# Performance work log

Measured on AMD Instinct MI355X. Metric: run time of the kernel, lower is better.

The kernel has to match this reference:

```python
import jax, jax.numpy as jnp
import numpy as np

B, N, F, H, D = 4096, 14, 768, 1, 768  # batch, num_diseases, feature_dim, num_heads, hidden_dim
L = 3  # number of GAT layers


def setup_inputs() -> dict:
    key = jax.random.key(0)
    ks = jax.random.split(key, 8)
    features = jax.random.normal(ks[0], (B, N, F), dtype=jnp.float32)
    # random adjacency mask; ensure nonzero diagonal so no row is fully masked
    mask = (jax.random.uniform(ks[1], (B, N, N)) > 0.3).astype(jnp.float32)
    adj = jnp.maximum(mask, jnp.eye(N, dtype=jnp.float32))
    W_emb = jax.random.normal(ks[2], (F, D), dtype=jnp.float32) / np.sqrt(F)
    b_emb = jnp.zeros((D,), dtype=jnp.float32)
    gat_W = jax.random.normal(ks[3], (L, D, H * D), dtype=jnp.float32) / np.sqrt(D)
    gat_a = jax.random.normal(ks[4], (L, 2 * D, H), dtype=jnp.float32) / np.sqrt(2 * D)
    W_out = jax.random.normal(ks[5], (H * D, F), dtype=jnp.float32) / np.sqrt(H * D)
    b_out = jnp.zeros((F,), dtype=jnp.float32)
    return dict(features=features, adj=adj, W_emb=W_emb, b_emb=b_emb,
                gat_W=gat_W, gat_a=gat_a, W_out=W_out, b_out=b_out)


def _gat_layer(x, adj, W, a):
    # x: [B, N, D], W: [D, H*D], a: [2D, H]
    Bm, Nn = x.shape[0], x.shape[1]
    Wh = (x @ W).reshape(Bm, Nn, H, D)
    # e[b,i,j,h] = Wh[b,i,h] . a[:D,h] + Wh[b,j,h] . a[D:,h]  (concat attention, un-materialized)
    a_i, a_j = a[:D], a[D:]
    ei = jnp.einsum('bnhd,dh->bnh', Wh, a_i)
    ej = jnp.einsum('bnhd,dh->bnh', Wh, a_j)
    e = ei[:, :, None, :] + ej[:, None, :, :]  # [B, N, N, H]
    e = jnp.where(adj[..., None] > 0, e, jnp.float32(-1e30))  # masked_fill(-inf)
    attn = jax.nn.softmax(e, axis=2)  # softmax over j (dim=2), matches torch
    h = jnp.einsum('bijh,bjhd->bihd', attn, Wh)  # attention-weighted aggregation
    return h.reshape(Bm, Nn, H * D), attn  # concat=True output


def reference(features, adj, W_emb, b_emb, gat_W, gat_a, W_out, b_out):
    # dropout layers are identity at inference
    x = features @ W_emb + b_emb  # disease_embedding
    attns = []
    for l in range(L):
        x, attn = _gat_layer(x, adj, gat_W[l], gat_a[l])
        attns.append(attn)
        if l < L - 1:
            x = jax.nn.elu(x)
    out = x @ W_out + b_out  # output_proj
    return (out, attns[0], attns[1], attns[2])
```

## Files before the change

kernel.cpp:

```cpp
#include <hip/hip_runtime.h>

typedef unsigned short u16;
typedef float f32x4 __attribute__((ext_vector_type(4)));
typedef float f32x16 __attribute__((ext_vector_type(16)));
typedef short bf16x8 __attribute__((ext_vector_type(8)));
typedef unsigned short u16x8 __attribute__((ext_vector_type(8)));

#define ND 768
#define KD 768

__device__ __forceinline__ float bf2f(u16 u) {
    union { unsigned i; float f; } v; v.i = ((unsigned)u) << 16; return v.f;
}
__device__ __forceinline__ u16 f2bf(float f) {
    union { float f; unsigned u; } x; x.f = f;
    unsigned r = x.u + 0x7fffu + ((x.u >> 16) & 1u);
    return (u16)(r >> 16);
}
__device__ __forceinline__ void async16(const void* g, void* l) {
    __builtin_amdgcn_global_load_lds((const __attribute__((address_space(1))) void*)g,
                                     (__attribute__((address_space(3))) void*)l, 16, 0, 0);
}

__global__ __launch_bounds__(256) void conv_w(const float* __restrict__ W_emb,
                                              const float* __restrict__ gat_W,
                                              const float* __restrict__ W_out,
                                              u16* __restrict__ Wt)
{
    __shared__ float lds[64][65];
    const int m  = blockIdx.x / 144;
    const int r  = blockIdx.x % 144;
    const int tr = r / 12;
    const int tc = r % 12;
    const float* src = (m == 0) ? W_emb : (m <= 3) ? (gat_W + (size_t)(m - 1) * 589824) : W_out;
    const int c  = threadIdx.x & 63;
    const int w4 = threadIdx.x >> 6;
    #pragma unroll
    for (int i = 0; i < 16; ++i) {
        int kk = i * 4 + w4;
        lds[kk][c] = src[(size_t)(tr * 64 + kk) * 768 + tc * 64 + c];
    }
    __syncthreads();
    u16* dst = Wt + (size_t)m * 589824;
    #pragma unroll
    for (int i = 0; i < 16; ++i) {
        int nn = i * 4 + w4;
        dst[(size_t)(tc * 64 + nn) * 768 + tr * 64 + c] = f2bf(lds[c][nn]);
    }
}

__global__ __launch_bounds__(256) void conv_w1(const float* __restrict__ src,
                                               u16* __restrict__ dst)
{
    __shared__ float lds[64][65];
    const int r  = blockIdx.x;
    const int tr = r / 12;
    const int tc = r % 12;
    const int c  = threadIdx.x & 63;
    const int w4 = threadIdx.x >> 6;
    #pragma unroll
    for (int i = 0; i < 16; ++i) {
        int kk = i * 4 + w4;
        lds[kk][c] = src[(size_t)(tr * 64 + kk) * 768 + tc * 64 + c];
    }
    __syncthreads();
    #pragma unroll
    for (int i = 0; i < 16; ++i) {
        int nn = i * 4 + w4;
        dst[(size_t)(tc * 64 + nn) * 768 + tr * 64 + c] = f2bf(lds[c][nn]);
    }
}

__global__ __launch_bounds__(256) void conv_x(const float4* __restrict__ in,
                                              u16* __restrict__ outp, int n4)
{
    for (int i = blockIdx.x * 256 + threadIdx.x; i < n4; i += gridDim.x * 256) {
        float4 v = in[i];
        union { u16 s[4]; uint2 u; } o;
        o.s[0] = f2bf(v.x); o.s[1] = f2bf(v.y); o.s[2] = f2bf(v.z); o.s[3] = f2bf(v.w);
        ((uint2*)outp)[i] = o.u;
    }
}

__global__ __launch_bounds__(256) void prep_vecs(const float* __restrict__ W3,
                                                 const float* __restrict__ ga2,
                                                 const float* __restrict__ be,
                                                 const u16* __restrict__ Wt1,
                                                 float* __restrict__ w3ai,
                                                 float* __restrict__ w3aj,
                                                 float* __restrict__ bfus)
{
    int d = blockIdx.x * 256 + threadIdx.x;
    if (d >= 768) return;
    const float* row = W3 + (size_t)d * 768;
    float ai = 0.f, aj = 0.f;
    for (int n = 0; n < 768; ++n) { float w = row[n]; ai += w * ga2[n]; aj += w * ga2[768 + n]; }
    w3ai[d] = ai; w3aj[d] = aj;
    const u16* wt = Wt1 + (size_t)d * 768;
    float bf = 0.f;
    for (int j = 0; j < 768; ++j) bf += be[j] * bf2f(wt[j]);
    bfus[d] = bf;
}

template<bool F32OUT, bool SWZ>
__global__ __launch_bounds__(256) void gemm_bt(const u16* __restrict__ A,
                                               const u16* __restrict__ Bt,
                                               const float* __restrict__ bias,
                                               void* __restrict__ Cout)
{
    __shared__ u16 lds2[2][2][4096];
    const int tid  = threadIdx.x;
    const int lane = tid & 63;
    const int wvb  = tid & ~63;
    const int wm   = ((tid >> 7) & 1) * 64;
    const int wn   = ((tid >> 6) & 1) * 64;
    const int wg = blockIdx.x;
    const int id = SWZ ? ((wg & 7) * 336 + (wg >> 3)) : wg;
    const int tn = (id % 6) * 128;
    const int tm = (id / 6) * 128;

    f32x16 acc[2][2] = {};

    const int r31 = lane & 31;
    const int l5  = lane >> 5;
    const int key = (r31 >> 1) & 3;

    const int row0 = tid >> 2;
    const int kc0  = (((tid & 3) ^ ((tid >> 3) & 3)) << 3);
    const u16* aSrc = A  + (size_t)(tm + row0) * KD + kc0;
    const u16* bSrc = Bt + (size_t)(tn + row0) * KD + kc0;

    #define STAGE(b, ks_) { const int k0 = (ks_) * 32;                      \
        async16(aSrc + k0,                  &lds2[b][0][wvb * 8]);          \
        async16(aSrc + (size_t)64 * KD + k0, &lds2[b][0][(256 + wvb) * 8]); \
        async16(bSrc + k0,                  &lds2[b][1][wvb * 8]);          \
        async16(bSrc + (size_t)64 * KD + k0, &lds2[b][1][(256 + wvb) * 8]); }

    STAGE(0, 0);

    #pragma unroll 2
    for (int ks = 0; ks < KD / 32; ++ks) {
        const int cur = ks & 1;
        if (ks + 1 < KD / 32) {
            STAGE(cur ^ 1, ks + 1);
            asm volatile("s_waitcnt vmcnt(4)" ::: "memory");
        } else {
            asm volatile("s_waitcnt vmcnt(0)" ::: "memory");
        }
        __builtin_amdgcn_s_barrier();
        asm volatile("" ::: "memory");

        const u16* As = lds2[cur][0];
        const u16* Bs = lds2[cur][1];
        bf16x8 af[2][2], bf[2][2];
        #pragma unroll
        for (int fr = 0; fr < 2; ++fr)
            #pragma unroll
            for (int ka = 0; ka < 2; ++ka) {
                int chA = ((ka * 2 + l5) ^ key) << 3;
                af[fr][ka] = *(const bf16x8*)&As[(wm + fr * 32 + r31) * 32 + chA];
                bf[fr][ka] = *(const bf16x8*)&Bs[(wn + fr * 32 + r31) * 32 + chA];
            }
        #pragma unroll
        for (int fr = 0; fr < 2; ++fr)
            #pragma unroll
            for (int fc = 0; fc < 2; ++fc)
                #pragma unroll
                for (int ka = 0; ka < 2; ++ka)
                    acc[fr][fc] = __builtin_amdgcn_mfma_f32_32x32x16_bf16(
                        af[fr][ka], bf[fc][ka], acc[fr][fc], 0, 0, 0);

        if (ks + 1 < KD / 32) {
            asm volatile("" ::: "memory");
            __builtin_amdgcn_s_barrier();
        }
    }
    #undef STAGE

    #pragma unroll
    for (int fc = 0; fc < 2; ++fc) {
        int col = tn + wn + fc * 32 + r31;
        float bv = bias ? bias[col] : 0.0f;
        #pragma unroll
        for (int fr = 0; fr < 2; ++fr) {
            int rowb = tm + wm + fr * 32 + 4 * l5;
            #pragma unroll
            for (int reg = 0; reg < 16; ++reg) {
                int row = rowb + (reg & 3) + 8 * (reg >> 2);
                float v = acc[fr][fc][reg] + bv;
                if (F32OUT)
                    ((float*)Cout)[(size_t)row * ND + col] = v;
                else
                    ((u16*)Cout)[(size_t)row * ND + col] = f2bf(v);
            }
        }
    }
}

template<bool ELU, bool DOTS>
__global__ __launch_bounds__(256) void gat_mix(const u16* __restrict__ Wh,
                                               const float* __restrict__ adj,
                                               const float* __restrict__ avec,
                                               float* __restrict__ attn_out,
                                               u16* __restrict__ Xout,
                                               const float* __restrict__ w3ai,
                                               const float* __restrict__ w3aj,
                                               float* __restrict__ eiOut,
                                               float* __restrict__ ejOut)
{
    __shared__ u16 wh[14 * 768];
    __shared__ float s_ei[14], s_ej[14];
    __shared__ float s_attn[196];
    __shared__ float s_dots[14][2];
    const int b = blockIdx.x;
    const int tid = threadIdx.x;
    const u16* whb = Wh + (size_t)b * 10752;

    if (DOTS && tid < 28) ((float*)s_dots)[tid] = 0.f;
    for (int c = tid; c < 1344; c += 256)
        ((uint4*)wh)[c] = ((const uint4*)whb)[c];
    __syncthreads();

    if (tid < 224) {
        const int i = tid >> 4, l = tid & 15;
        float ai = 0.f, aj = 0.f;
        #pragma unroll
        for (int c = 0; c < 6; ++c) {
            int d = c * 128 + l * 8;
            u16x8 v  = *(const u16x8*)&wh[i * 768 + d];
            float4 x0 = *(const float4*)&avec[d];
            float4 x1 = *(const float4*)&avec[d + 4];
            float4 y0 = *(const float4*)&avec[768 + d];
            float4 y1 = *(const float4*)&avec[768 + d + 4];
            float w0 = bf2f(v[0]), w1 = bf2f(v[1]), w2 = bf2f(v[2]), w3 = bf2f(v[3]);
            float w4 = bf2f(v[4]), w5 = bf2f(v[5]), w6 = bf2f(v[6]), w7 = bf2f(v[7]);
            ai += w0*x0.x + w1*x0.y + w2*x0.z + w3*x0.w + w4*x1.x + w5*x1.y + w6*x1.z + w7*x1.w;
            aj += w0*y0.x + w1*y0.y + w2*y0.z + w3*y0.w + w4*y1.x + w5*y1.y + w6*y1.z + w7*y1.w;
        }
        #pragma unroll
        for (int off = 8; off; off >>= 1) {
            ai += __shfl_xor(ai, off);
            aj += __shfl_xor(aj, off);
        }
        if (l == 0) { s_ei[i] = ai; s_ej[i] = aj; }
    }
    __syncthreads();

    if (tid < 14) {
        const int i = tid;
        float e[14];
        float mx = -3.0e38f;
        #pragma unroll
        for (int j = 0; j < 14; ++j) {
            float ev = (adj[(size_t)b * 196 + i * 14 + j] > 0.f) ? (s_ei[i] + s_ej[j]) : -1.0e30f;
            e[j] = ev; mx = fmaxf(mx, ev);
        }
        float sum = 0.f;
        #pragma unroll
        for (int j = 0; j < 14; ++j) { float pp = __expf(e[j] - mx); e[j] = pp; sum += pp; }
        float inv = 1.0f / sum;
        #pragma unroll
        for (int j = 0; j < 14; ++j) s_attn[i * 14 + j] = e[j] * inv;
    }
    __syncthreads();

    if (tid < 196) attn_out[(size_t)b * 196 + tid] = s_attn[tid];

    for (int pp = tid; pp < 14 * 48; pp += 256) {
        const int i  = pp / 48;
        const int d0 = (pp % 48) * 16;
        float acc[16] = {};
        #pragma unroll
        for (int j = 0; j < 14; ++j) {
            float aw = s_attn[i * 14 + j];
            u16x8 wv0 = *(const u16x8*)&wh[j * 768 + d0];
            u16x8 wv1 = *(const u16x8*)&wh[j * 768 + d0 + 8];
            #pragma unroll
            for (int qq = 0; qq < 8; ++qq) {
                acc[qq]     += aw * bf2f(wv0[qq]);
                acc[8 + qq] += aw * bf2f(wv1[qq]);
            }
        }
        float pi = 0.f, pj = 0.f;
        union { u16 s[16]; uint4 u[2]; } o;
        #pragma unroll
        for (int qq = 0; qq < 16; ++qq) {
            float v = acc[qq];
            if (ELU && v < 0.f) v = __expf(v) - 1.0f;
            if (DOTS) { pi += v * w3ai[d0 + qq]; pj += v * w3aj[d0 + qq]; }
            o.s[qq] = f2bf(v);
        }
        if (DOTS) {
            atomicAdd(&s_dots[i][0], pi);
            atomicAdd(&s_dots[i][1], pj);
        }
        *(uint4*)&Xout[(size_t)b * 10752 + i * 768 + d0]     = o.u[0];
        *(uint4*)&Xout[(size_t)b * 10752 + i * 768 + d0 + 8] = o.u[1];
    }
    if (DOTS) {
        __syncthreads();
        if (tid < 14) {
            eiOut[(size_t)b * 14 + tid] = s_dots[tid][0];
            ejOut[(size_t)b * 14 + tid] = s_dots[tid][1];
        }
    }
}

__global__ __launch_bounds__(256) void gat_out(const u16* __restrict__ Z,
                                               const float* __restrict__ adj,
                                               const float* __restrict__ eiG,
                                               const float* __restrict__ ejG,
                                               const float* __restrict__ b_out,
                                               float* __restrict__ attn_out,
                                               float* __restrict__ outp)
{
    __shared__ u16 wh[14 * 768];
    __shared__ float s_attn[196];
    const int b = blockIdx.x;
    const int tid = threadIdx.x;
    const u16* zb = Z + (size_t)b * 10752;

    for (int c = tid; c < 1344; c += 256)
        ((uint4*)wh)[c] = ((const uint4*)zb)[c];

    if (tid < 14) {
        const int i = tid;
        float ei = eiG[(size_t)b * 14 + i];
        float e[14];
        float mx = -3.0e38f;
        #pragma unroll
        for (int j = 0; j < 14; ++j) {
            float ev = (adj[(size_t)b * 196 + i * 14 + j] > 0.f)
                           ? (ei + ejG[(size_t)b * 14 + j]) : -1.0e30f;
            e[j] = ev; mx = fmaxf(mx, ev);
        }
        float sum = 0.f;
        #pragma unroll
        for (int j = 0; j < 14; ++j) { float pp = __expf(e[j] - mx); e[j] = pp; sum += pp; }
        float inv = 1.0f / sum;
        #pragma unroll
        for (int j = 0; j < 14; ++j) s_attn[i * 14 + j] = e[j] * inv;
    }
    __syncthreads();

    if (tid < 196) attn_out[(size_t)b * 196 + tid] = s_attn[tid];

    for (int pp = tid; pp < 14 * 48; pp += 256) {
        const int i  = pp / 48;
        const int d0 = (pp % 48) * 16;
        float acc[16];
        #pragma unroll
        for (int qq = 0; qq < 16; ++qq) acc[qq] = b_out[d0 + qq];
        #pragma unroll
        for (int j = 0; j < 14; ++j) {
            float aw = s_attn[i * 14 + j];
            u16x8 wv0 = *(const u16x8*)&wh[j * 768 + d0];
            u16x8 wv1 = *(const u16x8*)&wh[j * 768 + d0 + 8];
            #pragma unroll
            for (int qq = 0; qq < 8; ++qq) {
                acc[qq]     += aw * bf2f(wv0[qq]);
                acc[8 + qq] += aw * bf2f(wv1[qq]);
            }
        }
        float* dst = &outp[(size_t)b * 10752 + i * 768 + d0];
        *(float4*)(dst)      = *(float4*)&acc[0];
        *(float4*)(dst + 4)  = *(float4*)&acc[4];
        *(float4*)(dst + 8)  = *(float4*)&acc[8];
        *(float4*)(dst + 12) = *(float4*)&acc[12];
    }
}

extern "C" void kernel_launch(void* const* d_in, const int* in_sizes, int n_in,
                              void* d_out, int out_size, void* d_ws, size_t ws_size,
                              hipStream_t stream)
{
    const float* features = (const float*)d_in[0];
    const float* adj      = (const float*)d_in[1];
    const float* W_emb    = (const float*)d_in[2];
    const float* b_emb    = (const float*)d_in[3];
    const float* gat_W    = (const float*)d_in[4];
    const float* gat_a    = (const float*)d_in[5];
    const float* W_out    = (const float*)d_in[6];
    const float* b_out    = (const float*)d_in[7];
    float* out = (float*)d_out;

    u16* Wh = (u16*)d_ws;
    u16* Wt = Wh + 44040192;
    float* scr  = (float*)(Wt + 7 * 589824);
    float* w3ai = scr + 589824;
    float* w3aj = w3ai + 768;
    float* bfus = w3aj + 768;
    float* eiG  = bfus + 768;
    float* ejG  = eiG + 57344;
    u16* H0 = (u16*)d_out;
    u16* H1 = H0 + 44040192;
    u16* WeBf = H1;
    u16* W3Bf = H1 + 589824;
    float* attn0 = out + 44040192;
    float* attn1 = attn0 + 802816;
    float* attn2 = attn1 + 802816;

    conv_w<<<dim3(720), 256, 0, stream>>>(W_emb, gat_W, W_out, Wt);
    conv_x<<<dim3(4096), 256, 0, stream>>>((const float4*)features, H0, 11010048);
    conv_x<<<dim3(576), 256, 0, stream>>>((const float4*)W_emb, WeBf, 147456);
    conv_x<<<dim3(576), 256, 0, stream>>>((const float4*)(gat_W + 2 * 589824), W3Bf, 147456);
    prep_vecs<<<dim3(3), 256, 0, stream>>>(gat_W + 2 * 589824, gat_a + 2 * 1536, b_emb,
                                           Wt + 589824, w3ai, w3aj, bfus);
    gemm_bt<true, false><<<dim3(36), 256, 0, stream>>>(WeBf, Wt + 1 * 589824, nullptr, scr);
    conv_w1<<<dim3(144), 256, 0, stream>>>(scr, Wt + 5 * 589824);
    gemm_bt<true, false><<<dim3(36), 256, 0, stream>>>(W3Bf, Wt + 4 * 589824, nullptr, scr);
    conv_w1<<<dim3(144), 256, 0, stream>>>(scr, Wt + 6 * 589824);

    dim3 gg(2688);
    gemm_bt<false, true><<<gg, 256, 0, stream>>>(H0, Wt + 5 * 589824, bfus, Wh);
    gat_mix<true, false><<<dim3(4096), 256, 0, stream>>>(Wh, adj, gat_a, attn0, H1,
                                                         nullptr, nullptr, nullptr, nullptr);
    gemm_bt<false, true><<<gg, 256, 0, stream>>>(H1, Wt + 2 * 589824, nullptr, Wh);
    gat_mix<true, true><<<dim3(4096), 256, 0, stream>>>(Wh, adj, gat_a + 1536, attn1, H0,
                                                        w3ai, w3aj, eiG, ejG);
    gemm_bt<false, true><<<gg, 256, 0, stream>>>(H0, Wt + 6 * 589824, nullptr, Wh);
    gat_out<<<dim3(4096), 256, 0, stream>>>(Wh, adj, eiG, ejG, b_out, attn2, out);
}
```

Baseline: 661.7 us.

## Fuse feature fp32-to-bf16 conversion into first GEMM and batch weight precompute

The first big GEMM now reads the fp32 features directly. It converts them to bf16 in registers and writes them to LDS, which removes the separate conv_x pass over the 44M-element feature tensor and its bf16 write and re-read. The two small weight-product GEMMs and their transpose kernels are each merged into a single launch by choosing the B matrix per row tile. The cost is synchronous fp32 loads for A, with extra waits and register pressure in the main GEMM's pipeline.

```diff
diff --git a/kernel.cpp b/kernel.cpp
--- a/kernel.cpp
+++ b/kernel.cpp
@@ -49,13 +49,16 @@
     }
 }
 
-__global__ __launch_bounds__(256) void conv_w1(const float* __restrict__ src,
-                                               u16* __restrict__ dst)
+__global__ __launch_bounds__(256) void conv_w2(const float* __restrict__ src0,
+                                               u16* __restrict__ dst0)
 {
     __shared__ float lds[64][65];
-    const int r  = blockIdx.x;
+    const int m  = blockIdx.x / 144;
+    const int r  = blockIdx.x % 144;
     const int tr = r / 12;
     const int tc = r % 12;
+    const float* src = src0 + (size_t)m * 589824;
+    u16* dst = dst0 + (size_t)m * 589824;
     const int c  = threadIdx.x & 63;
     const int w4 = threadIdx.x >> 6;
     #pragma unroll
@@ -102,9 +105,10 @@
     bfus[d] = bf;
 }
 
-template<bool F32OUT, bool SWZ>
-__global__ __launch_bounds__(256) void gemm_bt(const u16* __restrict__ A,
+template<bool F32OUT, bool SWZ, bool A32>
+__global__ __launch_bounds__(256) void gemm_bt(const void* __restrict__ Ain,
                                                const u16* __restrict__ Bt,
+                                               const u16* __restrict__ Bt2,
                                                const float* __restrict__ bias,
                                                void* __restrict__ Cout)
 {
@@ -118,6 +122,7 @@
     const int id = SWZ ? ((wg & 7) * 336 + (wg >> 3)) : wg;
     const int tn = (id % 6) * 128;
     const int tm = (id / 6) * 128;
+    const u16* BtU = (Bt2 != nullptr && tm >= 768) ? Bt2 : Bt;
 
     f32x16 acc[2][2] = {};
 
@@ -127,26 +132,58 @@
 
     const int row0 = tid >> 2;
     const int kc0  = (((tid & 3) ^ ((tid >> 3) & 3)) << 3);
-    const u16* aSrc = A  + (size_t)(tm + row0) * KD + kc0;
-    const u16* bSrc = Bt + (size_t)(tn + row0) * KD + kc0;
-
-    #define STAGE(b, ks_) { const int k0 = (ks_) * 32;                      \
-        async16(aSrc + k0,                  &lds2[b][0][wvb * 8]);          \
-        async16(aSrc + (size_t)64 * KD + k0, &lds2[b][0][(256 + wvb) * 8]); \
-        async16(bSrc + k0,                  &lds2[b][1][wvb * 8]);          \
+    const u16*   aS16 = (const u16*)Ain  + (size_t)(tm + row0) * KD + kc0;
+    const float* aS32 = (const float*)Ain + (size_t)(tm + row0) * KD + kc0;
+    const u16*   bSrc = BtU + (size_t)(tn + row0) * KD + kc0;
+
+    #define STAGE_B16(b, ks_) { const int k0 = (ks_) * 32;                   \
+        async16(bSrc + k0,                   &lds2[b][1][wvb * 8]);          \
         async16(bSrc + (size_t)64 * KD + k0, &lds2[b][1][(256 + wvb) * 8]); }
-
-    STAGE(0, 0);
+    #define STAGE_A16(b, ks_) { const int k0 = (ks_) * 32;                   \
+        async16(aS16 + k0,                   &lds2[b][0][wvb * 8]);          \
+        async16(aS16 + (size_t)64 * KD + k0, &lds2[b][0][(256 + wvb) * 8]); }
+    #define LOADA32(ks_) { const int k0 = (ks_) * 32;                        \
+        ar0 = *(const float4*)(aS32 + k0);                                   \
+        ar1 = *(const float4*)(aS32 + k0 + 4);                               \
+        ar2 = *(const float4*)(aS32 + (size_t)64 * KD + k0);                 \
+        ar3 = *(const float4*)(aS32 + (size_t)64 * KD + k0 + 4); }
+    #define WRA32(b) { union { u16 s[8]; uint4 u; } p0, p1;                  \
+        p0.s[0]=f2bf(ar0.x); p0.s[1]=f2bf(ar0.y); p0.s[2]=f2bf(ar0.z); p0.s[3]=f2bf(ar0.w); \
+        p0.s[4]=f2bf(ar1.x); p0.s[5]=f2bf(ar1.y); p0.s[6]=f2bf(ar1.z); p0.s[7]=f2bf(ar1.w); \
+        p1.s[0]=f2bf(ar2.x); p1.s[1]=f2bf(ar2.y); p1.s[2]=f2bf(ar2.z); p1.s[3]=f2bf(ar2.w); \
+        p1.s[4]=f2bf(ar3.x); p1.s[5]=f2bf(ar3.y); p1.s[6]=f2bf(ar3.z); p1.s[7]=f2bf(ar3.w); \
+        *(uint4*)&lds2[b][0][(size_t)tid * 8]         = p0.u;                \
+        *(uint4*)&lds2[b][0][(size_t)(256 + tid) * 8] = p1.u; }
+
+    float4 ar0, ar1, ar2, ar3;
+
+    if (A32) {
+        LOADA32(0);
+        STAGE_B16(0, 0);
+        asm volatile("s_waitcnt vmcnt(2)" ::: "memory");
+        WRA32(0);
+    } else {
+        STAGE_A16(0, 0);
+        STAGE_B16(0, 0);
+    }
 
     #pragma unroll 2
     for (int ks = 0; ks < KD / 32; ++ks) {
         const int cur = ks & 1;
         if (ks + 1 < KD / 32) {
-            STAGE(cur ^ 1, ks + 1);
-            asm volatile("s_waitcnt vmcnt(4)" ::: "memory");
+            if (A32) {
+                LOADA32(ks + 1);
+                STAGE_B16(cur ^ 1, ks + 1);
+                asm volatile("s_waitcnt vmcnt(6)" ::: "memory");
+            } else {
+                STAGE_A16(cur ^ 1, ks + 1);
+                STAGE_B16(cur ^ 1, ks + 1);
+                asm volatile("s_waitcnt vmcnt(4)" ::: "memory");
+            }
         } else {
             asm volatile("s_waitcnt vmcnt(0)" ::: "memory");
         }
+        if (A32) asm volatile("s_waitcnt lgkmcnt(0)" ::: "memory");
         __builtin_amdgcn_s_barrier();
         asm volatile("" ::: "memory");
 
@@ -171,11 +208,19 @@
                         af[fr][ka], bf[fc][ka], acc[fr][fc], 0, 0, 0);
 
         if (ks + 1 < KD / 32) {
+            if (A32) {
+                asm volatile("s_waitcnt vmcnt(2)" ::: "memory");
+                WRA32(cur ^ 1);
+            }
             asm volatile("" ::: "memory");
             __builtin_amdgcn_s_barrier();
-        }
-    }
-    #undef STAGE
+            asm volatile("" ::: "memory");
+        }
+    }
+    #undef STAGE_A16
+    #undef STAGE_B16
+    #undef LOADA32
+    #undef WRA32
 
     #pragma unroll
     for (int fc = 0; fc < 2; ++fc) {
@@ -387,37 +432,37 @@
     u16* Wh = (u16*)d_ws;
     u16* Wt = Wh + 44040192;
     float* scr  = (float*)(Wt + 7 * 589824);
-    float* w3ai = scr + 589824;
+    float* w3ai = scr + 1179648;
     float* w3aj = w3ai + 768;
     float* bfus = w3aj + 768;
     float* eiG  = bfus + 768;
     float* ejG  = eiG + 57344;
     u16* H0 = (u16*)d_out;
     u16* H1 = H0 + 44040192;
-    u16* WeBf = H1;
-    u16* W3Bf = H1 + 589824;
+    u16* WeW3 = H0;
     float* attn0 = out + 44040192;
     float* attn1 = attn0 + 802816;
     float* attn2 = attn1 + 802816;
 
     conv_w<<<dim3(720), 256, 0, stream>>>(W_emb, gat_W, W_out, Wt);
-    conv_x<<<dim3(4096), 256, 0, stream>>>((const float4*)features, H0, 11010048);
-    conv_x<<<dim3(576), 256, 0, stream>>>((const float4*)W_emb, WeBf, 147456);
-    conv_x<<<dim3(576), 256, 0, stream>>>((const float4*)(gat_W + 2 * 589824), W3Bf, 147456);
+    conv_x<<<dim3(576), 256, 0, stream>>>((const float4*)W_emb, WeW3, 147456);
+    conv_x<<<dim3(576), 256, 0, stream>>>((const float4*)(gat_W + 2 * 589824), WeW3 + 589824, 147456);
     prep_vecs<<<dim3(3), 256, 0, stream>>>(gat_W + 2 * 589824, gat_a + 2 * 1536, b_emb,
                                            Wt + 589824, w3ai, w3aj, bfus);
-    gemm_bt<true, false><<<dim3(36), 256, 0, stream>>>(WeBf, Wt + 1 * 589824, nullptr, scr);
-    conv_w1<<<dim3(144), 256, 0, stream>>>(scr, Wt + 5 * 589824);
-    gemm_bt<true, false><<<dim3(36), 256, 0, stream>>>(W3Bf, Wt + 4 * 589824, nullptr, scr);
-    conv_w1<<<dim3(144), 256, 0, stream>>>(scr, Wt + 6 * 589824);
+    gemm_bt<true, false, false><<<dim3(72), 256, 0, stream>>>(
+        WeW3, Wt + 1 * 589824, Wt + 4 * 589824, nullptr, scr);
+    conv_w2<<<dim3(288), 256, 0, stream>>>(scr, Wt + 5 * 589824);
 
     dim3 gg(2688);
-    gemm_bt<false, true><<<gg, 256, 0, stream>>>(H0, Wt + 5 * 589824, bfus, Wh);
-    gat_mix<true, false><<<dim3(4096), 256, 0, stream>>>(Wh, adj, gat_a, attn0, H1,
+    gemm_bt<false, true, true><<<gg, 256, 0, stream>>>(
+        features, Wt + 5 * 589824, nullptr, bfus, Wh);
+    gat_mix<true, false><<<dim3(4096), 256, 0, stream>>>(Wh, adj, gat_a, attn0, H0,
                                                          nullptr, nullptr, nullptr, nullptr);
-    gemm_bt<false, true><<<gg, 256, 0, stream>>>(H1, Wt + 2 * 589824, nullptr, Wh);
-    gat_mix<true, true><<<dim3(4096), 256, 0, stream>>>(Wh, adj, gat_a + 1536, attn1, H0,
+    gemm_bt<false, true, false><<<gg, 256, 0, stream>>>(
+        H0, Wt + 2 * 589824, nullptr, nullptr, Wh);
+    gat_mix<true, true><<<dim3(4096), 256, 0, stream>>>(Wh, adj, gat_a + 1536, attn1, H1,
                                                         w3ai, w3aj, eiG, ejG);
-    gemm_bt<false, true><<<gg, 256, 0, stream>>>(H0, Wt + 6 * 589824, nullptr, Wh);
+    gemm_bt<false, true, false><<<gg, 256, 0, stream>>>(
+        H1, Wt + 6 * 589824, nullptr, nullptr, Wh);
     gat_out<<<dim3(4096), 256, 0, stream>>>(Wh, adj, eiG, ejG, b_out, attn2, out);
 }
```

Measured after the change: 659.9 us. No clear change (-0.3%).
